# Optimization experiments

Measured on AMD Instinct MI355X. Metric: run time of the kernel, lower is better.

Reference implementation:

```python
import jax, jax.numpy as jnp
import numpy as np

B, NODES, VOCAB, EMB, GIN_DIM, E_PER = 4096, 32, 100, 64, 64, 512
N = B * NODES            # total nodes in batched graph
LN_EPS = 1e-5


def setup_inputs() -> dict:
    key = jax.random.key(0)
    ks = jax.random.split(key, 12)
    x = jax.random.randint(ks[0], (B, NODES - 1), 0, VOCAB)
    los = jax.random.randint(ks[1], (B,), 0, 37)
    # intra-graph edges with per-graph node offsets -> flat batched edge_index [2, B*E_PER]
    src = jax.random.randint(ks[2], (B, E_PER), 0, NODES)
    dst = jax.random.randint(ks[3], (B, E_PER), 0, NODES)
    off = (jnp.arange(B) * NODES)[:, None]
    edge_index = jnp.stack([(src + off).reshape(-1), (dst + off).reshape(-1)])

    def w(k, shape, fan_in):
        return jax.random.normal(k, shape, dtype=jnp.float32) / np.float32(np.sqrt(fan_in))

    emb_tables = w(ks[4], (NODES, VOCAB, EMB), 1.0)  # one table per node/column
    win1 = w(ks[5], (EMB, GIN_DIM), EMB); bin1 = jnp.zeros((GIN_DIM,), jnp.float32)
    gin_g = jnp.ones((GIN_DIM,), jnp.float32); gin_b = jnp.zeros((GIN_DIM,), jnp.float32)
    win2 = w(ks[6], (GIN_DIM, GIN_DIM), GIN_DIM); bin2 = jnp.zeros((GIN_DIM,), jnp.float32)
    # hidden GIN MLP is SHARED across hidden layers (torch code reuses one nn.Sequential)
    wh1 = w(ks[7], (GIN_DIM, GIN_DIM), GIN_DIM); bh1 = jnp.zeros((GIN_DIM,), jnp.float32)
    gh_g = jnp.ones((GIN_DIM,), jnp.float32); gh_b = jnp.zeros((GIN_DIM,), jnp.float32)
    wh2 = w(ks[8], (GIN_DIM, GIN_DIM), GIN_DIM); bh2 = jnp.zeros((GIN_DIM,), jnp.float32)
    eps = jnp.zeros((3,), jnp.float32)  # trainable eps per layer, init 0
    cdim = GIN_DIM * 3
    wc1 = w(ks[9], (cdim, cdim * 2), cdim); bc1 = jnp.zeros((cdim * 2,), jnp.float32)
    wc2 = w(ks[10], (cdim * 2, 1), cdim * 2); bc2 = jnp.zeros((1,), jnp.float32)
    return dict(x=x, los=los, edge_index=edge_index, emb_tables=emb_tables,
                win1=win1, bin1=bin1, gin_g=gin_g, gin_b=gin_b, win2=win2, bin2=bin2,
                wh1=wh1, bh1=bh1, gh_g=gh_g, gh_b=gh_b, wh2=wh2, bh2=bh2,
                eps=eps, wc1=wc1, bc1=bc1, wc2=wc2, bc2=bc2)


def _ln(z, g, b):
    mu = z.mean(-1, keepdims=True)
    var = ((z - mu) ** 2).mean(-1, keepdims=True)
    return (z - mu) * jax.lax.rsqrt(var + LN_EPS) * g + b


def _gin_layer(h, src, dst, eps, W1, b1, g, be, W2, b2):
    # sum-aggregate neighbors: out_i = (1+eps)*h_i + sum_{(j,i) in E} h_j
    agg = jax.ops.segment_sum(h[src], dst, num_segments=N)
    z = (1.0 + eps) * h + agg
    z = jax.nn.relu(_ln(z @ W1 + b1, g, be))
    return z @ W2 + b2


def reference(x, los, edge_index, emb_tables, win1, bin1, gin_g, gin_b, win2, bin2,
              wh1, bh1, gh_g, gh_b, wh2, bh2, eps, wc1, bc1, wc2, bc2):
    xf = jnp.concatenate([x, los[:, None]], axis=1)        # [B, NODES]
    h = emb_tables[jnp.arange(NODES)[None, :], xf]         # per-column embedding lookup -> [B, NODES, EMB]
    h = h.reshape(N, EMB)
    src, dst = edge_index[0], edge_index[1]
    h1 = _gin_layer(h, src, dst, eps[0], win1, bin1, gin_g, gin_b, win2, bin2)
    h2 = _gin_layer(h1, src, dst, eps[1], wh1, bh1, gh_g, gh_b, wh2, bh2)
    h3 = _gin_layer(h2, src, dst, eps[2], wh1, bh1, gh_g, gh_b, wh2, bh2)
    pooled = jnp.concatenate([t.reshape(B, NODES, -1).sum(axis=1) for t in (h1, h2, h3)], axis=1)  # [B, 192]
    return jax.nn.relu(pooled @ wc1 + bc1) @ wc2 + bc2     # [B, 1]
```

## Files before the change

### kernel.cpp

```cpp
#include <hip/hip_runtime.h>

#define NBATCH 4096
#define NNODE  32
#define NVOCAB 100
#define DIM    64
#define EPG    512
#define HSTR   68
#define LN_EPS 1e-5f
#define CDIM   192
#define C2DIM  384
#define GWORDS 2304

#define WS_WFRAG_OFF   0
#define WS_B21_OFF     49152
#define WS_WCF_OFF     65536
#define WS_BCE_OFF     360448
#define WS_POOL_OFF    364544

typedef float          f32x4  __attribute__((ext_vector_type(4)));
typedef unsigned int   u32x4  __attribute__((ext_vector_type(4)));
typedef __bf16         bf16x8 __attribute__((ext_vector_type(8)));

__device__ __forceinline__ float4 ldg4(const float* __restrict__ p) {
    return *reinterpret_cast<const float4*>(p);
}
__device__ __forceinline__ unsigned short f2bf(float f) {
    return __builtin_bit_cast(unsigned short, static_cast<__bf16>(f));
}
__device__ __forceinline__ float bf2f(unsigned short h) {
    return static_cast<float>(__builtin_bit_cast(__bf16, h));
}
__device__ __forceinline__ unsigned int pk2(float a, float b) {
    return (unsigned int)f2bf(a) | ((unsigned int)f2bf(b) << 16);
}
__device__ __forceinline__ unsigned int pk2lo(float a, float b, unsigned int hi) {
    const float ra = a - bf2f((unsigned short)(hi & 0xffff));
    const float rb = b - bf2f((unsigned short)(hi >> 16));
    return pk2(ra, rb);
}
__device__ __forceinline__ bf16x8 as_bf(u32x4 v) {
    return __builtin_bit_cast(bf16x8, v);
}
__device__ __forceinline__ float rowsum16(float v) {
    int x = __builtin_bit_cast(int, v);
    v += __builtin_bit_cast(float, __builtin_amdgcn_update_dpp(0, x, 0x128, 0xF, 0xF, false));
    x = __builtin_bit_cast(int, v);
    v += __builtin_bit_cast(float, __builtin_amdgcn_update_dpp(0, x, 0x124, 0xF, 0xF, false));
    x = __builtin_bit_cast(int, v);
    v += __builtin_bit_cast(float, __builtin_amdgcn_update_dpp(0, x, 0x122, 0xF, 0xF, false));
    x = __builtin_bit_cast(int, v);
    v += __builtin_bit_cast(float, __builtin_amdgcn_update_dpp(0, x, 0x121, 0xF, 0xF, false));
    return v;
}
#define MFMA(a, b, c) __builtin_amdgcn_mfma_f32_16x16x32_bf16(as_bf(a), as_bf(b), (c), 0, 0, 0)

extern "C" __global__ void __launch_bounds__(256)
prep_w_kernel(const float* __restrict__ win1, const float* __restrict__ win2,
              const float* __restrict__ wh1,  const float* __restrict__ wh2,
              const float* __restrict__ wc1,  const float* __restrict__ bin2,
              const float* __restrict__ bh2,  const float* __restrict__ bc1,
              unsigned short* __restrict__ wsb, unsigned short* __restrict__ wcf,
              float* __restrict__ b21, float* __restrict__ bce)
{
    __shared__ float sh[14400];
    const int blk = blockIdx.x, t = threadIdx.x;

    if (blk < 3) {
        float* C = sh + 4096;
        if (blk == 0) {
            for (int i = t; i < 1024; i += 256)
                *(float4*)&C[i * 4] = ldg4(win1 + i * 4);
            __syncthreads();
        } else {
            const float* A2 = (blk == 1) ? win2 : wh2;
            const float* bb = (blk == 1) ? bin2 : bh2;
            float* Bm    = sh;
            float* A2lds = sh + 8192;
            for (int i = t; i < 1024; i += 256)
                *(float4*)&Bm[i * 4] = ldg4(wh1 + i * 4);
            for (int i = t; i < 4096; i += 256) {
                const int r = i >> 6, k = i & 63;
                A2lds[r * 65 + k] = A2[i];
            }
            __syncthreads();
            const int r = t >> 2, cb = (t & 3) * 16;
            float av[16];
            #pragma unroll
            for (int c = 0; c < 16; ++c) av[c] = 0.f;
            for (int k = 0; k < 64; ++k) {
                const float a = A2lds[r * 65 + k];
                const float4 w0 = *(const float4*)&Bm[k * 64 + cb];
                const float4 w1 = *(const float4*)&Bm[k * 64 + cb + 4];
                const float4 w2 = *(const float4*)&Bm[k * 64 + cb + 8];
                const float4 w3 = *(const float4*)&Bm[k * 64 + cb + 12];
                av[0]=fmaf(a,w0.x,av[0]); av[1]=fmaf(a,w0.y,av[1]); av[2]=fmaf(a,w0.z,av[2]); av[3]=fmaf(a,w0.w,av[3]);
                av[4]=fmaf(a,w1.x,av[4]); av[5]=fmaf(a,w1.y,av[5]); av[6]=fmaf(a,w1.z,av[6]); av[7]=fmaf(a,w1.w,av[7]);
                av[8]=fmaf(a,w2.x,av[8]); av[9]=fmaf(a,w2.y,av[9]); av[10]=fmaf(a,w2.z,av[10]); av[11]=fmaf(a,w2.w,av[11]);
                av[12]=fmaf(a,w3.x,av[12]); av[13]=fmaf(a,w3.y,av[13]); av[14]=fmaf(a,w3.z,av[14]); av[15]=fmaf(a,w3.w,av[15]);
            }
            #pragma unroll
            for (int c = 0; c < 16; ++c) C[r * 64 + cb + c] = av[c];
            if (t < 64) {
                float s = 0.f;
                for (int k = 0; k < 64; ++k) s = fmaf(bb[k], Bm[k * 64 + t], s);
                b21[(blk - 1) * 64 + t] = s;
            }
            __syncthreads();
        }
        unsigned short* hi = wsb + blk * 8192;
        unsigned short* lo = hi + 4096;
        for (int f = t; f < 512; f += 256) {
            const int s = f >> 8, n = (f >> 6) & 3, ll = f & 63;
            const int g = ll >> 4, col = n * 16 + (ll & 15);
            unsigned int uh[4], ul[4];
            #pragma unroll
            for (int j2 = 0; j2 < 4; ++j2) {
                const float a  = C[(s * 32 + g * 8 + j2 * 2)     * 64 + col];
                const float bq = C[(s * 32 + g * 8 + j2 * 2 + 1) * 64 + col];
                uh[j2] = pk2(a, bq);
                ul[j2] = pk2lo(a, bq, uh[j2]);
            }
            *(u32x4*)(hi + f * 8) = (u32x4){uh[0], uh[1], uh[2], uh[3]};
            *(u32x4*)(lo + f * 8) = (u32x4){ul[0], ul[1], ul[2], ul[3]};
        }
    } else if (blk < 15) {
        const int chunk = blk - 3;
        float* wc1c = sh;
        float* A2T  = sh + 6144;
        for (int i = t; i < 1536; i += 256) {
            const int row = i >> 3, q = i & 7;
            *(float4*)&wc1c[row * 32 + q * 4] = ldg4(wc1 + (size_t)row * C2DIM + chunk * 32 + q * 4);
        }
        for (int i = t; i < 8192; i += 256) {
            const int r = i >> 6, k = i & 63;
            const float v = (r < 64) ? win2[r * 64 + k] : wh2[(r - 64) * 64 + k];
            A2T[k * 129 + r] = v;
        }
        __syncthreads();
        float acc[32];
        if (t < 192) {
            const int R  = (t < 64) ? t : 64 + (t & 63);
            const int kb = (t >> 6) * 64;
            #pragma unroll
            for (int c = 0; c < 32; ++c) acc[c] = 0.f;
            for (int k = 0; k < 64; ++k) {
                const float a = A2T[k * 129 + R];
                const float* wr = &wc1c[(kb + k) * 32];
                #pragma unroll
                for (int c4 = 0; c4 < 8; ++c4) {
                    const float4 w = *(const float4*)&wr[c4 * 4];
                    acc[c4 * 4 + 0] = fmaf(a, w.x, acc[c4 * 4 + 0]);
                    acc[c4 * 4 + 1] = fmaf(a, w.y, acc[c4 * 4 + 1]);
                    acc[c4 * 4 + 2] = fmaf(a, w.z, acc[c4 * 4 + 2]);
                    acc[c4 * 4 + 3] = fmaf(a, w.w, acc[c4 * 4 + 3]);
                }
            }
        }
        __syncthreads();
        float* C2 = sh;
        if (t < 192) {
            #pragma unroll
            for (int c = 0; c < 32; ++c) C2[t * 33 + c] = acc[c];
        }
        __syncthreads();
        unsigned short* hi = wcf;
        unsigned short* lo = wcf + 73728;
        for (int i = t; i < 768; i += 256) {
            const int s = i / 128, rem = i % 128;
            const int nl = rem >> 6, ll = rem & 63;
            const int n = chunk * 2 + nl;
            const int e = (s * 24 + n) * 64 + ll;
            const int cl = nl * 16 + (ll & 15);
            const int k0 = s * 32 + (ll >> 4) * 8;
            unsigned int uh[4], ul[4];
            #pragma unroll
            for (int j2 = 0; j2 < 4; ++j2) {
                const float a  = C2[(k0 + j2 * 2)     * 33 + cl];
                const float bq = C2[(k0 + j2 * 2 + 1) * 33 + cl];
                uh[j2] = pk2(a, bq);
                ul[j2] = pk2lo(a, bq, uh[j2]);
            }
            *(u32x4*)(hi + e * 8) = (u32x4){uh[0], uh[1], uh[2], uh[3]};
            *(u32x4*)(lo + e * 8) = (u32x4){ul[0], ul[1], ul[2], ul[3]};
        }
    } else {
        for (int j = t; j < C2DIM; j += 256) {
            float s = 0.f;
            for (int k = 0; k < 64; ++k) {
                s = fmaf(bin2[k], wc1[(size_t)k * C2DIM + j], s);
                s = fmaf(bh2[k],  wc1[(size_t)(64 + k) * C2DIM + j], s);
                s = fmaf(bh2[k],  wc1[(size_t)(128 + k) * C2DIM + j], s);
            }
            bce[j] = bc1[j] + 32.0f * s;
        }
    }
}

extern "C" __global__ void __launch_bounds__(256, 4)
gin_fused_kernel(const int* __restrict__ x, const int* __restrict__ los,
                 const int* __restrict__ eidx,
                 const float* __restrict__ emb,
                 const float* __restrict__ bin1,
                 const float* __restrict__ gin_g, const float* __restrict__ gin_b,
                 const float* __restrict__ bh1,
                 const float* __restrict__ gh_g, const float* __restrict__ gh_b,
                 const float* __restrict__ epsv,
                 const unsigned short* __restrict__ wsb,
                 const float* __restrict__ b21,
                 float* __restrict__ pooled_ws)
{
    __shared__ __align__(16) float S[4 * GWORDS];

    const int t  = threadIdx.x;
    const int wv = t >> 6;
    const int l  = t & 63;
    const int b  = blockIdx.x * 4 + wv;
    float* scr = &S[wv * GWORDS];
    unsigned int* bp = (unsigned int*)scr;
    const int lc = l & 15;
    const int lg = l >> 4;

    int* cnt = (int*)scr;
    #pragma unroll
    for (int i = 0; i < 16; ++i) cnt[l + 64 * i] = 0;
    {
        const int ebase = b * EPG;
        const int goff  = b * NNODE;
        #pragma unroll
        for (int i = 0; i < 8; ++i) {
            const int e = ebase + l + 64 * i;
            const int sN = eidx[e] - goff;
            const int dN = eidx[NBATCH * EPG + e] - goff;
            atomicAdd(&cnt[dN * NNODE + sN], 1);
        }
    }
    u32x4 adjf[2];
    #pragma unroll
    for (int m = 0; m < 2; ++m) {
        const int4 a0 = *(const int4*)&cnt[(m * 16 + lc) * NNODE + lg * 8];
        const int4 a1 = *(const int4*)&cnt[(m * 16 + lc) * NNODE + lg * 8 + 4];
        adjf[m] = (u32x4){ pk2((float)a0.x, (float)a0.y), pk2((float)a0.z, (float)a0.w),
                           pk2((float)a1.x, (float)a1.y), pk2((float)a1.z, (float)a1.w) };
    }
    {
        const int node = l >> 1;
        const int idx = (node < NNODE - 1) ? x[b * (NNODE - 1) + node] : los[b];
        const float* er = emb + ((size_t)(node * NVOCAB + idx)) * DIM + (l & 1) * 32;
        float* sr = scr + node * HSTR + (l & 1) * 32;
        #pragma unroll
        for (int i = 0; i < 8; ++i)
            *reinterpret_cast<float4*>(sr + i * 4) = ldg4(er + i * 4);
    }

    f32x4 acc[2][4];
    u32x4 azh[2][2], azl[2][2];

    for (int st = 0; st < 3; ++st) {
        const unsigned short* Wf = wsb + st * 8192;
        const float* bpost = st ? bh1  : bin1;
        const float* Gg    = st ? gh_g : gin_g;
        const float* Gb    = st ? gh_b : gin_b;
        const float sc = 1.0f + epsv[st];

        if (st) {
            #pragma unroll
            for (int m = 0; m < 2; ++m)
                #pragma unroll
                for (int n = 0; n < 4; ++n)
                    #pragma unroll
                    for (int r = 0; r < 4; ++r)
                        scr[(m * 16 + lg * 4 + r) * HSTR + n * 16 + lc] = acc[m][n][r];
        }
        #pragma unroll
        for (int m = 0; m < 2; ++m)
            #pragma unroll
            for (int s = 0; s < 2; ++s) {
                const float4 v0 = *(const float4*)&scr[(m * 16 + lc) * HSTR + s * 32 + lg * 8];
                const float4 v1 = *(const float4*)&scr[(m * 16 + lc) * HSTR + s * 32 + lg * 8 + 4];
                azh[m][s] = (u32x4){ pk2(v0.x,v0.y), pk2(v0.z,v0.w), pk2(v1.x,v1.y), pk2(v1.z,v1.w) };
                azl[m][s] = (u32x4){ pk2lo(v0.x,v0.y,azh[m][s][0]), pk2lo(v0.z,v0.w,azh[m][s][1]),
                                     pk2lo(v1.x,v1.y,azh[m][s][2]), pk2lo(v1.z,v1.w,azh[m][s][3]) };
            }
        #pragma unroll
        for (int n = 0; n < 4; ++n) {
            const float bpv = st ? b21[(st - 1) * 64 + n * 16 + lc] : 0.f;
            #pragma unroll
            for (int m = 0; m < 2; ++m)
                acc[m][n] = (f32x4){bpv, bpv, bpv, bpv};
        }
        #pragma unroll
        for (int n = 0; n < 4; ++n)
            #pragma unroll
            for (int s = 0; s < 2; ++s) {
                const u32x4 wh = *(const u32x4*)(Wf +        ((s * 4 + n) * 64 + l) * 8);
                const u32x4 wl = *(const u32x4*)(Wf + 4096 + ((s * 4 + n) * 64 + l) * 8);
                #pragma unroll
                for (int m = 0; m < 2; ++m) {
                    acc[m][n] = MFMA(azh[m][s], wh, acc[m][n]);
                    acc[m][n] = MFMA(azh[m][s], wl, acc[m][n]);
                    acc[m][n] = MFMA(azl[m][s], wh, acc[m][n]);
                }
            }
        #pragma unroll
        for (int m = 0; m < 2; ++m)
            #pragma unroll
            for (int n = 0; n < 4; ++n) {
                const int col = n * 16 + lc;
                const int p0  = m * 8 + lg * 2;
                uint2 h2, l2;
                h2.x = pk2(acc[m][n][0], acc[m][n][1]);
                h2.y = pk2(acc[m][n][2], acc[m][n][3]);
                l2.x = pk2lo(acc[m][n][0], acc[m][n][1], h2.x);
                l2.y = pk2lo(acc[m][n][2], acc[m][n][3], h2.y);
                *(uint2*)&bp[col * 18 + p0]        = h2;
                *(uint2*)&bp[1152 + col * 18 + p0] = l2;
            }
        #pragma unroll
        for (int n = 0; n < 4; ++n) {
            const float bq = bpost[n * 16 + lc];
            #pragma unroll
            for (int m = 0; m < 2; ++m)
                #pragma unroll
                for (int r = 0; r < 4; ++r)
                    acc[m][n][r] = sc * acc[m][n][r] + bq;
        }
        #pragma unroll
        for (int n = 0; n < 4; ++n) {
            const int base = (n * 16 + lc) * 18 + lg * 4;
            const uint2 ha = *(const uint2*)&bp[base];
            const uint2 hb = *(const uint2*)&bp[base + 2];
            const uint2 la = *(const uint2*)&bp[1152 + base];
            const uint2 lb = *(const uint2*)&bp[1152 + base + 2];
            const u32x4 hh = (u32x4){ha.x, ha.y, hb.x, hb.y};
            const u32x4 hl = (u32x4){la.x, la.y, lb.x, lb.y};
            #pragma unroll
            for (int m = 0; m < 2; ++m) {
                acc[m][n] = MFMA(adjf[m], hh, acc[m][n]);
                acc[m][n] = MFMA(adjf[m], hl, acc[m][n]);
            }
        }
        {
            float gg[4], gb[4];
            #pragma unroll
            for (int n = 0; n < 4; ++n) { gg[n] = Gg[n * 16 + lc]; gb[n] = Gb[n * 16 + lc]; }
            #pragma unroll
            for (int m = 0; m < 2; ++m)
                #pragma unroll
                for (int r = 0; r < 4; ++r) {
                    float a0 = acc[m][0][r], a1 = acc[m][1][r];
                    float a2 = acc[m][2][r], a3 = acc[m][3][r];
                    const float s1 = rowsum16(a0 + a1 + a2 + a3);
                    const float s2 = rowsum16(a0 * a0 + a1 * a1 + a2 * a2 + a3 * a3);
                    const float mu  = s1 * (1.0f / 64.0f);
                    const float var = s2 * (1.0f / 64.0f) - mu * mu;
                    const float inv = rsqrtf(var + LN_EPS);
                    acc[m][0][r] = fmaxf((a0 - mu) * inv * gg[0] + gb[0], 0.f);
                    acc[m][1][r] = fmaxf((a1 - mu) * inv * gg[1] + gb[1], 0.f);
                    acc[m][2][r] = fmaxf((a2 - mu) * inv * gg[2] + gb[2], 0.f);
                    acc[m][3][r] = fmaxf((a3 - mu) * inv * gg[3] + gb[3], 0.f);
                }
        }
        #pragma unroll
        for (int n = 0; n < 4; ++n) {
            float p = 0.f;
            #pragma unroll
            for (int m = 0; m < 2; ++m)
                #pragma unroll
                for (int r = 0; r < 4; ++r) p += acc[m][n][r];
            p += __shfl_xor(p, 16);
            p += __shfl_xor(p, 32);
            if (l < 16)
                pooled_ws[(size_t)b * CDIM + st * DIM + n * 16 + l] = p;
        }
    }
}

extern "C" __global__ void __launch_bounds__(512)
classifier_kernel(const float* __restrict__ pooled_ws,
                  const unsigned short* __restrict__ wcf,
                  const float* __restrict__ bce, const float* __restrict__ wc2,
                  const float* __restrict__ bc2, float* __restrict__ out)
{
    #define PSTR 196
    __shared__ __align__(16) float P[16 * PSTR];
    __shared__ __align__(16) unsigned int afh[6 * 64 * 4];
    __shared__ __align__(16) unsigned int afl[6 * 64 * 4];
    __shared__ float rsum[8][16];

    const int b = blockIdx.x;
    const int t = threadIdx.x;
    const int l = t & 63;
    const int w = t >> 6;
    const unsigned short* wclo = wcf + 73728;

    for (int i = t; i < 16 * 48; i += 512) {
        const int row = i / 48, q = i % 48;
        const float4 v = ldg4(pooled_ws + ((size_t)(b * 16 + row)) * CDIM + q * 4);
        *reinterpret_cast<float4*>(&P[row * PSTR + q * 4]) = v;
    }
    __syncthreads();

    for (int e = t; e < 6 * 64; e += 512) {
        const int s = e >> 6, ll = e & 63;
        const int row = ll & 15;
        const int k0 = s * 32 + (ll >> 4) * 8;
        const float4 v0 = *reinterpret_cast<const float4*>(&P[row * PSTR + k0]);
        const float4 v1 = *reinterpret_cast<const float4*>(&P[row * PSTR + k0 + 4]);
        const float y[8] = { v0.x, v0.y, v0.z, v0.w, v1.x, v1.y, v1.z, v1.w };
        unsigned int uh[4], ul[4];
        #pragma unroll
        for (int j2 = 0; j2 < 4; ++j2) {
            uh[j2] = pk2(y[j2 * 2], y[j2 * 2 + 1]);
            ul[j2] = pk2lo(y[j2 * 2], y[j2 * 2 + 1], uh[j2]);
        }
        *reinterpret_cast<u32x4*>(&afh[e * 4]) = (u32x4){uh[0], uh[1], uh[2], uh[3]};
        *reinterpret_cast<u32x4*>(&afl[e * 4]) = (u32x4){ul[0], ul[1], ul[2], ul[3]};
    }
    __syncthreads();

    float part[4] = {0.f, 0.f, 0.f, 0.f};
    for (int nt = 0; nt < 3; ++nt) {
        const int n = w * 3 + nt;
        f32x4 acc = {0.f, 0.f, 0.f, 0.f};
        #pragma unroll
        for (int s = 0; s < 6; ++s) {
            const u32x4 ah = *(const u32x4*)&afh[(s * 64 + l) * 4];
            const u32x4 al = *(const u32x4*)&afl[(s * 64 + l) * 4];
            const u32x4 bh = *(const u32x4*)&wcf [((s * 24 + n) * 64 + l) * 8];
            const u32x4 bl = *(const u32x4*)&wclo[((s * 24 + n) * 64 + l) * 8];
            acc = MFMA(ah, bh, acc);
            acc = MFMA(ah, bl, acc);
            acc = MFMA(al, bh, acc);
        }
        const int col = n * 16 + (l & 15);
        const float bias = bce[col], w2 = wc2[col];
        #pragma unroll
        for (int r = 0; r < 4; ++r)
            part[r] += fmaxf(acc[r] + bias, 0.f) * w2;
    }
    #pragma unroll
    for (int r = 0; r < 4; ++r) {
        part[r] += __shfl_xor(part[r], 1);
        part[r] += __shfl_xor(part[r], 2);
        part[r] += __shfl_xor(part[r], 4);
        part[r] += __shfl_xor(part[r], 8);
    }
    if ((l & 15) == 0) {
        const int g = l >> 4;
        #pragma unroll
        for (int r = 0; r < 4; ++r) rsum[w][g * 4 + r] = part[r];
    }
    __syncthreads();
    if (t < 16) {
        float s = bc2[0];
        #pragma unroll
        for (int w2i = 0; w2i < 8; ++w2i) s += rsum[w2i][t];
        out[b * 16 + t] = s;
    }
}

extern "C" void kernel_launch(void* const* d_in, const int* in_sizes, int n_in,
                              void* d_out, int out_size, void* d_ws, size_t ws_size,
                              hipStream_t stream)
{
    const int*   x     = (const int*)d_in[0];
    const int*   los   = (const int*)d_in[1];
    const int*   eidx  = (const int*)d_in[2];
    const float* emb   = (const float*)d_in[3];
    const float* win1  = (const float*)d_in[4];
    const float* bin1  = (const float*)d_in[5];
    const float* gin_g = (const float*)d_in[6];
    const float* gin_b = (const float*)d_in[7];
    const float* win2  = (const float*)d_in[8];
    const float* bin2  = (const float*)d_in[9];
    const float* wh1   = (const float*)d_in[10];
    const float* bh1   = (const float*)d_in[11];
    const float* gh_g  = (const float*)d_in[12];
    const float* gh_b  = (const float*)d_in[13];
    const float* wh2   = (const float*)d_in[14];
    const float* bh2   = (const float*)d_in[15];
    const float* epsv  = (const float*)d_in[16];
    const float* wc1   = (const float*)d_in[17];
    const float* bc1   = (const float*)d_in[18];
    const float* wc2   = (const float*)d_in[19];
    const float* bc2   = (const float*)d_in[20];
    float* out = (float*)d_out;

    unsigned short* wsb = (unsigned short*)((char*)d_ws + WS_WFRAG_OFF);
    float*          b21 = (float*)((char*)d_ws + WS_B21_OFF);
    unsigned short* wcf = (unsigned short*)((char*)d_ws + WS_WCF_OFF);
    float*          bce = (float*)((char*)d_ws + WS_BCE_OFF);
    float*          cs  = (float*)((char*)d_ws + WS_POOL_OFF);

    hipLaunchKernelGGL(prep_w_kernel, dim3(16), dim3(256), 0, stream,
                       win1, win2, wh1, wh2, wc1, bin2, bh2, bc1,
                       wsb, wcf, b21, bce);
    hipLaunchKernelGGL(gin_fused_kernel, dim3(NBATCH / 4), dim3(256), 0, stream,
                       x, los, eidx, emb, bin1, gin_g, gin_b,
                       bh1, gh_g, gh_b, epsv,
                       (const unsigned short*)wsb, (const float*)b21, cs);
    hipLaunchKernelGGL(classifier_kernel, dim3(NBATCH / 16), dim3(512), 0, stream,
                       (const float*)cs, (const unsigned short*)wcf,
                       (const float*)bce, wc2, bc2, out);
}
```

Before: 54.17 us.

## Precompute embedding tables times first GIN weight and skip stage-0 matmul

The first GIN layer's input projection is linear, so the prep kernel now computes emb_tables @ win1 for all 3200 table rows in fp32 using 100 extra blocks. The fused kernel gathers the already-projected rows straight into the MFMA accumulators for stage 0. This removes the LDS staging, the bf16 hi/lo split and the three-way MFMA product for that stage. In exchange it adds prep work, an extra workspace buffer, and a scalar strided gather from that buffer instead of float4 embedding loads.

```diff
diff --git a/kernel.cpp b/kernel.cpp
--- a/kernel.cpp
+++ b/kernel.cpp
@@ -16,6 +16,7 @@
 #define WS_WCF_OFF     65536
 #define WS_BCE_OFF     360448
 #define WS_POOL_OFF    364544
+#define WS_EMBW_OFF    3510272
 
 typedef float          f32x4  __attribute__((ext_vector_type(4)));
 typedef unsigned int   u32x4  __attribute__((ext_vector_type(4)));
@@ -59,8 +60,10 @@
               const float* __restrict__ wh1,  const float* __restrict__ wh2,
               const float* __restrict__ wc1,  const float* __restrict__ bin2,
               const float* __restrict__ bh2,  const float* __restrict__ bc1,
+              const float* __restrict__ emb,
               unsigned short* __restrict__ wsb, unsigned short* __restrict__ wcf,
-              float* __restrict__ b21, float* __restrict__ bce)
+              float* __restrict__ b21, float* __restrict__ bce,
+              float* __restrict__ embw)
 {
     __shared__ float sh[14400];
     const int blk = blockIdx.x, t = threadIdx.x;
@@ -183,7 +186,7 @@
             *(u32x4*)(hi + e * 8) = (u32x4){uh[0], uh[1], uh[2], uh[3]};
             *(u32x4*)(lo + e * 8) = (u32x4){ul[0], ul[1], ul[2], ul[3]};
         }
-    } else {
+    } else if (blk == 15) {
         for (int j = t; j < C2DIM; j += 256) {
             float s = 0.f;
             for (int k = 0; k < 64; ++k) {
@@ -193,13 +196,44 @@
             }
             bce[j] = bc1[j] + 32.0f * s;
         }
+    } else {
+        const int rbase = (blk - 16) * 32;
+        float* W1l = sh;
+        float* er  = sh + 4096;
+        for (int i = t; i < 1024; i += 256)
+            *(float4*)&W1l[i * 4] = ldg4(win1 + i * 4);
+        for (int i = t; i < 512; i += 256) {
+            const int rr = i >> 4, q = i & 15;
+            const float4 v = ldg4(emb + (size_t)(rbase + rr) * 64 + q * 4);
+            er[rr * 65 + q * 4 + 0] = v.x;
+            er[rr * 65 + q * 4 + 1] = v.y;
+            er[rr * 65 + q * 4 + 2] = v.z;
+            er[rr * 65 + q * 4 + 3] = v.w;
+        }
+        __syncthreads();
+        const int rr = t >> 3, cg = (t & 7) * 8;
+        float a8[8];
+        #pragma unroll
+        for (int c = 0; c < 8; ++c) a8[c] = 0.f;
+        for (int k = 0; k < 64; ++k) {
+            const float a = er[rr * 65 + k];
+            const float4 w0 = *(const float4*)&W1l[k * 64 + cg];
+            const float4 w1 = *(const float4*)&W1l[k * 64 + cg + 4];
+            a8[0] = fmaf(a, w0.x, a8[0]); a8[1] = fmaf(a, w0.y, a8[1]);
+            a8[2] = fmaf(a, w0.z, a8[2]); a8[3] = fmaf(a, w0.w, a8[3]);
+            a8[4] = fmaf(a, w1.x, a8[4]); a8[5] = fmaf(a, w1.y, a8[5]);
+            a8[6] = fmaf(a, w1.z, a8[6]); a8[7] = fmaf(a, w1.w, a8[7]);
+        }
+        float* outr = embw + (size_t)(rbase + rr) * 64 + cg;
+        *(float4*)outr       = (float4){a8[0], a8[1], a8[2], a8[3]};
+        *(float4*)(outr + 4) = (float4){a8[4], a8[5], a8[6], a8[7]};
     }
 }
 
 extern "C" __global__ void __launch_bounds__(256, 4)
 gin_fused_kernel(const int* __restrict__ x, const int* __restrict__ los,
                  const int* __restrict__ eidx,
-                 const float* __restrict__ emb,
+                 const float* __restrict__ embw,
                  const float* __restrict__ bin1,
                  const float* __restrict__ gin_g, const float* __restrict__ gin_b,
                  const float* __restrict__ bh1,
@@ -242,27 +276,29 @@
         adjf[m] = (u32x4){ pk2((float)a0.x, (float)a0.y), pk2((float)a0.z, (float)a0.w),
                            pk2((float)a1.x, (float)a1.y), pk2((float)a1.z, (float)a1.w) };
     }
-    {
-        const int node = l >> 1;
-        const int idx = (node < NNODE - 1) ? x[b * (NNODE - 1) + node] : los[b];
-        const float* er = emb + ((size_t)(node * NVOCAB + idx)) * DIM + (l & 1) * 32;
-        float* sr = scr + node * HSTR + (l & 1) * 32;
-        #pragma unroll
-        for (int i = 0; i < 8; ++i)
-            *reinterpret_cast<float4*>(sr + i * 4) = ldg4(er + i * 4);
-    }
 
     f32x4 acc[2][4];
-    u32x4 azh[2][2], azl[2][2];
 
     for (int st = 0; st < 3; ++st) {
-        const unsigned short* Wf = wsb + st * 8192;
         const float* bpost = st ? bh1  : bin1;
         const float* Gg    = st ? gh_g : gin_g;
         const float* Gb    = st ? gh_b : gin_b;
         const float sc = 1.0f + epsv[st];
 
-        if (st) {
+        if (st == 0) {
+            #pragma unroll
+            for (int m = 0; m < 2; ++m)
+                #pragma unroll
+                for (int r = 0; r < 4; ++r) {
+                    const int node = m * 16 + lg * 4 + r;
+                    const int idx = (node < NNODE - 1) ? x[b * (NNODE - 1) + node] : los[b];
+                    const float* vr = embw + ((size_t)(node * NVOCAB + idx)) * DIM + lc;
+                    #pragma unroll
+                    for (int n = 0; n < 4; ++n)
+                        acc[m][n][r] = vr[n * 16];
+                }
+        } else {
+            const unsigned short* Wf = wsb + st * 8192;
             #pragma unroll
             for (int m = 0; m < 2; ++m)
                 #pragma unroll
@@ -270,37 +306,38 @@
                     #pragma unroll
                     for (int r = 0; r < 4; ++r)
                         scr[(m * 16 + lg * 4 + r) * HSTR + n * 16 + lc] = acc[m][n][r];
-        }
-        #pragma unroll
-        for (int m = 0; m < 2; ++m)
-            #pragma unroll
-            for (int s = 0; s < 2; ++s) {
-                const float4 v0 = *(const float4*)&scr[(m * 16 + lc) * HSTR + s * 32 + lg * 8];
-                const float4 v1 = *(const float4*)&scr[(m * 16 + lc) * HSTR + s * 32 + lg * 8 + 4];
-                azh[m][s] = (u32x4){ pk2(v0.x,v0.y), pk2(v0.z,v0.w), pk2(v1.x,v1.y), pk2(v1.z,v1.w) };
-                azl[m][s] = (u32x4){ pk2lo(v0.x,v0.y,azh[m][s][0]), pk2lo(v0.z,v0.w,azh[m][s][1]),
-                                     pk2lo(v1.x,v1.y,azh[m][s][2]), pk2lo(v1.z,v1.w,azh[m][s][3]) };
-            }
-        #pragma unroll
-        for (int n = 0; n < 4; ++n) {
-            const float bpv = st ? b21[(st - 1) * 64 + n * 16 + lc] : 0.f;
+            u32x4 azh[2][2], azl[2][2];
             #pragma unroll
             for (int m = 0; m < 2; ++m)
-                acc[m][n] = (f32x4){bpv, bpv, bpv, bpv};
-        }
-        #pragma unroll
-        for (int n = 0; n < 4; ++n)
-            #pragma unroll
-            for (int s = 0; s < 2; ++s) {
-                const u32x4 wh = *(const u32x4*)(Wf +        ((s * 4 + n) * 64 + l) * 8);
-                const u32x4 wl = *(const u32x4*)(Wf + 4096 + ((s * 4 + n) * 64 + l) * 8);
-                #pragma unroll
-                for (int m = 0; m < 2; ++m) {
-                    acc[m][n] = MFMA(azh[m][s], wh, acc[m][n]);
-                    acc[m][n] = MFMA(azh[m][s], wl, acc[m][n]);
-                    acc[m][n] = MFMA(azl[m][s], wh, acc[m][n]);
+                #pragma unroll
+                for (int s = 0; s < 2; ++s) {
+                    const float4 v0 = *(const float4*)&scr[(m * 16 + lc) * HSTR + s * 32 + lg * 8];
+                    const float4 v1 = *(const float4*)&scr[(m * 16 + lc) * HSTR + s * 32 + lg * 8 + 4];
+                    azh[m][s] = (u32x4){ pk2(v0.x,v0.y), pk2(v0.z,v0.w), pk2(v1.x,v1.y), pk2(v1.z,v1.w) };
+                    azl[m][s] = (u32x4){ pk2lo(v0.x,v0.y,azh[m][s][0]), pk2lo(v0.z,v0.w,azh[m][s][1]),
+                                         pk2lo(v1.x,v1.y,azh[m][s][2]), pk2lo(v1.z,v1.w,azh[m][s][3]) };
                 }
-            }
+            #pragma unroll
+            for (int n = 0; n < 4; ++n) {
+                const float bpv = b21[(st - 1) * 64 + n * 16 + lc];
+                #pragma unroll
+                for (int m = 0; m < 2; ++m)
+                    acc[m][n] = (f32x4){bpv, bpv, bpv, bpv};
+            }
+            #pragma unroll
+            for (int n = 0; n < 4; ++n)
+                #pragma unroll
+                for (int s = 0; s < 2; ++s) {
+                    const u32x4 wh = *(const u32x4*)(Wf +        ((s * 4 + n) * 64 + l) * 8);
+                    const u32x4 wl = *(const u32x4*)(Wf + 4096 + ((s * 4 + n) * 64 + l) * 8);
+                    #pragma unroll
+                    for (int m = 0; m < 2; ++m) {
+                        acc[m][n] = MFMA(azh[m][s], wh, acc[m][n]);
+                        acc[m][n] = MFMA(azh[m][s], wl, acc[m][n]);
+                        acc[m][n] = MFMA(azl[m][s], wh, acc[m][n]);
+                    }
+                }
+        }
         #pragma unroll
         for (int m = 0; m < 2; ++m)
             #pragma unroll
@@ -491,12 +528,13 @@
     unsigned short* wcf = (unsigned short*)((char*)d_ws + WS_WCF_OFF);
     float*          bce = (float*)((char*)d_ws + WS_BCE_OFF);
     float*          cs  = (float*)((char*)d_ws + WS_POOL_OFF);
-
-    hipLaunchKernelGGL(prep_w_kernel, dim3(16), dim3(256), 0, stream,
-                       win1, win2, wh1, wh2, wc1, bin2, bh2, bc1,
-                       wsb, wcf, b21, bce);
+    float*          embw= (float*)((char*)d_ws + WS_EMBW_OFF);
+
+    hipLaunchKernelGGL(prep_w_kernel, dim3(116), dim3(256), 0, stream,
+                       win1, win2, wh1, wh2, wc1, bin2, bh2, bc1, emb,
+                       wsb, wcf, b21, bce, embw);
     hipLaunchKernelGGL(gin_fused_kernel, dim3(NBATCH / 4), dim3(256), 0, stream,
-                       x, los, eidx, emb, bin1, gin_g, gin_b,
+                       x, los, eidx, (const float*)embw, bin1, gin_g, gin_b,
                        bh1, gh_g, gh_b, epsv,
                        (const unsigned short*)wsb, (const float*)b21, cs);
     hipLaunchKernelGGL(classifier_kernel, dim3(NBATCH / 16), dim3(512), 0, stream,
```

After: 50.16 us, median of 2. -7.4%, faster.
